# Kernel tuning notes

Hardware: AMD Instinct MI355X
Metric: run time of the kernel (lower is better)

The kernel has to match this reference:

```python
import jax, jax.numpy as jnp
import numpy as np

N = 4096
INPUT_DIM = 256
HIDDEN = 64
HEADS = 8
NEG_SLOPE = 0.2
MASK_FILL = -10000.0


def setup_inputs() -> dict:
    key = jax.random.key(0)
    k_x, k_adj, k_w, k_as, k_ad = jax.random.split(key, 5)
    x = jax.random.normal(k_x, (N, INPUT_DIM), dtype=jnp.float32)
    adjacency = jax.random.bernoulli(k_adj, 0.05, (N, N)) | jnp.eye(N, dtype=bool)
    # linear weight, torch convention: [out_features, in_features]
    W = jax.random.normal(k_w, (HEADS * HIDDEN, INPUT_DIM), dtype=jnp.float32) * 0.05
    attn_src = jax.random.normal(k_as, (HEADS, HIDDEN), dtype=jnp.float32) * 0.1
    attn_dst = jax.random.normal(k_ad, (HEADS, HIDDEN), dtype=jnp.float32) * 0.1
    return {"x": x, "adjacency": adjacency, "W": W, "attn_src": attn_src, "attn_dst": attn_dst}


def reference(x, adjacency, W, attn_src, attn_dst):
    # h: [N, heads, hidden]
    h = (x @ W.T).reshape(N, HEADS, HIDDEN)
    src_scores = jnp.einsum('nhd,hd->nh', h, attn_src)  # [N, heads]
    dst_scores = jnp.einsum('nhd,hd->nh', h, attn_dst)  # [N, heads]
    # logits[i, j, h] = src[i, h] + dst[j, h]  (matches torch permute(2,0,1) layout math)
    logits = src_scores[:, None, :] + dst_scores[None, :, :]  # [N, N, heads]
    logits = jax.nn.leaky_relu(logits, negative_slope=NEG_SLOPE)
    logits = jnp.where(adjacency[:, :, None], logits, MASK_FILL)
    alpha = jax.nn.softmax(logits, axis=1)  # softmax over source nodes j
    out = jnp.einsum('ijh,jhf->ihf', alpha, h)  # [N, heads, hidden]
    return out.mean(axis=1)  # [N, hidden]
```

## Files before the change

### kernel.cpp

```cpp
#include <hip/hip_runtime.h>

#define NN 4096
#define IN_DIM 256
#define HID 64
#define HEADS 8

typedef __attribute__((ext_vector_type(4))) float f32x4;
typedef __attribute__((ext_vector_type(8))) short s16x8;
typedef unsigned short u16;
typedef unsigned long long u64;

__device__ inline u16 f2bf(float f) {
  union { float f; unsigned u; } v; v.f = f;
  unsigned r = (v.u + 0x7FFFu + ((v.u >> 16) & 1u)) >> 16;
  return (u16)r;
}
__device__ inline float bf2f(u16 b) {
  union { unsigned u; float f; } v; v.u = ((unsigned)b) << 16;
  return v.f;
}
__device__ __forceinline__ unsigned cvt_pk_bf16(float a, float b) {
  unsigned r;
  asm("v_cvt_pk_bf16_f32 %0, %1, %2" : "=v"(r) : "v"(a), "v"(b));
  return r;
}

__global__ __launch_bounds__(256) void gat_pack(
    const void* __restrict__ adj, u64* __restrict__ bits)
{
  __shared__ int smode;
  const int t = threadIdx.x;
  if (t < 64) {
    const unsigned char* a8 = (const unsigned char*)adj;
    const int* a32 = (const int*)adj;
    size_t i8 = (size_t)(4 * t + 1) * 4097;
    int p8 = a8[i8] != 0;
    size_t k = (size_t)(2 * t + 1);
    int p32 = a32[k * 4097] != 0;
    int p64 = a32[2 * k * 4097] != 0;
    int ok8 = __all(p8), ok32 = __all(p32), ok64 = __all(p64);
    if (t == 0) smode = ok8 ? 0 : (ok32 ? 1 : (ok64 ? 2 : 1));
  }
  __syncthreads();
  const int mode = smode;

  const int lane = t & 63;
  const int wave = (blockIdx.x * blockDim.x + t) >> 6;
  const int nwaves = (gridDim.x * blockDim.x) >> 6;
  const size_t nwords = (size_t)NN * NN / 64;

  for (size_t w = wave; w < nwords; w += nwaves) {
    size_t e = w * 64 + lane;
    int on;
    if (mode == 1)      on = ((const int*)adj)[e] != 0;
    else if (mode == 0) on = ((const unsigned char*)adj)[e] != 0;
    else                on = ((const long long*)adj)[e] != 0;
    u64 b = __ballot(on);
    if (lane == 0) bits[w] = b;
  }
}

__global__ __launch_bounds__(256) void gat_gemm1(
    const float* __restrict__ x, const float* __restrict__ W,
    const float* __restrict__ a_src, const float* __restrict__ a_dst,
    u16* __restrict__ Hbt, float* __restrict__ s_srcT,
    float* __restrict__ s_dstT)
{
  __shared__ u16 xhi[64 * 72], xlo[64 * 72], whi[64 * 72], wlo[64 * 72];
  const int nb = blockIdx.x;
  const int ob = blockIdx.y;
  const int t = threadIdx.x;
  const int lane = t & 63, wid = t >> 6;
  const int wr = wid >> 1, wc = wid & 1;
  const int g = lane >> 4;

  f32x4 acc[2][2] = {};

  const int sn = t >> 2;
  const int skc = (t & 3) * 16;

  for (int kb = 0; kb < 4; ++kb) {
    const float* xr = x + (size_t)(nb * 64 + sn) * IN_DIM + kb * 64 + skc;
    const float* wr_p = W + (size_t)(ob * 64 + sn) * IN_DIM + kb * 64 + skc;
#pragma unroll
    for (int c = 0; c < 4; ++c) {
      float4 xv = ((const float4*)xr)[c];
      float4 wv = ((const float4*)wr_p)[c];
      float xf[4] = {xv.x, xv.y, xv.z, xv.w};
      float wf[4] = {wv.x, wv.y, wv.z, wv.w};
      u16 xh[4], xl[4], wh[4], wl[4];
#pragma unroll
      for (int e = 0; e < 4; ++e) {
        xh[e] = f2bf(xf[e]); xl[e] = f2bf(xf[e] - bf2f(xh[e]));
        wh[e] = f2bf(wf[e]); wl[e] = f2bf(wf[e] - bf2f(wh[e]));
      }
      int base = sn * 72 + skc + c * 4;
      *(ushort4*)(xhi + base) = make_ushort4(xh[0], xh[1], xh[2], xh[3]);
      *(ushort4*)(xlo + base) = make_ushort4(xl[0], xl[1], xl[2], xl[3]);
      *(ushort4*)(whi + base) = make_ushort4(wh[0], wh[1], wh[2], wh[3]);
      *(ushort4*)(wlo + base) = make_ushort4(wl[0], wl[1], wl[2], wl[3]);
    }
    __syncthreads();
#pragma unroll
    for (int ks = 0; ks < 2; ++ks) {
      const int k0 = ks * 32 + g * 8;
      s16x8 ah[2], al[2], bh[2], bl[2];
#pragma unroll
      for (int nf = 0; nf < 2; ++nf) {
        int row = wr * 32 + nf * 16 + (lane & 15);
        ah[nf] = *(const s16x8*)(xhi + row * 72 + k0);
        al[nf] = *(const s16x8*)(xlo + row * 72 + k0);
      }
#pragma unroll
      for (int of = 0; of < 2; ++of) {
        int row = wc * 32 + of * 16 + (lane & 15);
        bh[of] = *(const s16x8*)(whi + row * 72 + k0);
        bl[of] = *(const s16x8*)(wlo + row * 72 + k0);
      }
#pragma unroll
      for (int nf = 0; nf < 2; ++nf)
#pragma unroll
        for (int of = 0; of < 2; ++of) {
          acc[nf][of] = __builtin_amdgcn_mfma_f32_16x16x32_bf16(ah[nf], bh[of], acc[nf][of], 0, 0, 0);
          acc[nf][of] = __builtin_amdgcn_mfma_f32_16x16x32_bf16(ah[nf], bl[of], acc[nf][of], 0, 0, 0);
          acc[nf][of] = __builtin_amdgcn_mfma_f32_16x16x32_bf16(al[nf], bh[of], acc[nf][of], 0, 0, 0);
        }
    }
    __syncthreads();
  }

  u16* Ct = xhi;
#pragma unroll
  for (int nf = 0; nf < 2; ++nf)
#pragma unroll
    for (int of = 0; of < 2; ++of)
#pragma unroll
      for (int r = 0; r < 4; ++r) {
        int nloc = wr * 32 + nf * 16 + g * 4 + r;
        int oloc = wc * 32 + of * 16 + (lane & 15);
        Ct[oloc * 72 + nloc] = f2bf(acc[nf][of][r]);
      }

  {
    const float* asp = a_src + ob * 64;
    const float* adp = a_dst + ob * 64;
    float as0 = asp[wc * 32 + (lane & 15)], as1 = asp[wc * 32 + 16 + (lane & 15)];
    float ad0 = adp[wc * 32 + (lane & 15)], ad1 = adp[wc * 32 + 16 + (lane & 15)];
    float* sred = (float*)wlo;
#pragma unroll
    for (int nf = 0; nf < 2; ++nf)
#pragma unroll
      for (int r = 0; r < 4; ++r) {
        float vs = acc[nf][0][r] * as0 + acc[nf][1][r] * as1;
        float vd = acc[nf][0][r] * ad0 + acc[nf][1][r] * ad1;
#pragma unroll
        for (int m = 1; m < 16; m <<= 1) { vs += __shfl_xor(vs, m); vd += __shfl_xor(vd, m); }
        if ((lane & 15) == 0) {
          int node = wr * 32 + nf * 16 + g * 4 + r;
          sred[wc * 64 + node] = vs;
          sred[128 + wc * 64 + node] = vd;
        }
      }
  }
  __syncthreads();
  {
    int o = t >> 2, nc = (t & 3) * 16;
    u16* dst = Hbt + ((size_t)(ob * 64 + nb) * 64 + o) * 64 + nc;
#pragma unroll
    for (int c = 0; c < 2; ++c) {
      s16x8 v = *(const s16x8*)(Ct + o * 72 + nc + c * 8);
      *(s16x8*)(dst + c * 8) = v;
    }
  }
  if (t < 64) {
    const float* sred = (const float*)wlo;
    s_srcT[(size_t)ob * NN + nb * 64 + t] = sred[t] + sred[64 + t];
    s_dstT[(size_t)ob * NN + nb * 64 + t] = sred[128 + t] + sred[192 + t];
  }
}

__global__ __launch_bounds__(512) void gat_dmax(
    const float* __restrict__ s_dstT, float* __restrict__ Mh)
{
  const int w = threadIdx.x >> 6, lane = threadIdx.x & 63;
  const float* p = s_dstT + (size_t)w * NN;
  float m = -INFINITY;
#pragma unroll
  for (int it = 0; it < 16; ++it) {
    f32x4 v = *(const f32x4*)(p + (it * 64 + lane) * 4);
    m = fmaxf(fmaxf(fmaxf(m, v[0]), v[1]), fmaxf(v[2], v[3]));
  }
#pragma unroll
  for (int s = 1; s < 64; s <<= 1) m = fmaxf(m, __shfl_xor(m, s));
  if (lane == 0) Mh[w] = m;
}

__global__ __launch_bounds__(512, 4) void gat_flash(
    const u64* __restrict__ bits, const u16* __restrict__ Hbt,
    const float* __restrict__ s_srcT, const float* __restrict__ s_dstT,
    const float* __restrict__ Mh, float* __restrict__ pout)
{
  __shared__ char shmem[32768];
  __shared__ float Lbuf[8][16];
  u16* Ast = (u16*)shmem;

  const int t = threadIdx.x, lane = t & 63, wid = t >> 6;
  const int ws4 = wid & 3, jh = wid >> 2;
  const int bid = blockIdx.x;
  const int h = bid & 7, iblk = bid >> 3;
  const int i_loc = lane & 15, g = lane >> 4, j0 = g * 8;
  const int irow = iblk * 64 + ws4 * 16 + i_loc;

  const float s_i = s_srcT[(size_t)h * NN + irow];
  float m_i = s_i + Mh[h];
  m_i = fmaxf(m_i, 0.2f * m_i);
  const float L2E = 1.44269504f;
  const float mL = m_i * L2E;

  const u16* tile0 = Hbt + (size_t)h * 64 * 4096;
  const float* dT = s_dstT + (size_t)h * NN;
  const u64* brow = bits + (size_t)irow * 64;

  const int lt = t & 255;
  const int r0 = lt >> 3, colE = (lt & 7) * 8;
  const u16* gsrc0 = tile0 + r0 * 64 + (colE ^ ((r0 & 7) << 3));
  const u16* gsrc1 = tile0 + (32 + r0) * 64 + (colE ^ ((r0 & 7) << 3));
  u16* sgrp = Ast + jh * 8192;
  const int swz = (i_loc & 7) << 4;

  f32x4 acc[4] = {};
  f32x4 lacc = {0.f, 0.f, 0.f, 0.f};

#define QUAD(DV, MBITS, SH, PW0, PW1, LI) do {                        \
    float z0 = s_i + DV[0], z1 = s_i + DV[1];                         \
    float z2 = s_i + DV[2], z3 = s_i + DV[3];                         \
    z0 = fmaxf(z0, 0.2f * z0); z1 = fmaxf(z1, 0.2f * z1);             \
    z2 = fmaxf(z2, 0.2f * z2); z3 = fmaxf(z3, 0.2f * z3);             \
    float e0 = __builtin_amdgcn_exp2f(__builtin_fmaf(z0, L2E, -mL));  \
    float e1 = __builtin_amdgcn_exp2f(__builtin_fmaf(z1, L2E, -mL));  \
    float e2 = __builtin_amdgcn_exp2f(__builtin_fmaf(z2, L2E, -mL));  \
    float e3 = __builtin_amdgcn_exp2f(__builtin_fmaf(z3, L2E, -mL));  \
    e0 = ((MBITS >> (SH + 0)) & 1u) ? e0 : 0.f;                       \
    e1 = ((MBITS >> (SH + 1)) & 1u) ? e1 : 0.f;                       \
    e2 = ((MBITS >> (SH + 2)) & 1u) ? e2 : 0.f;                       \
    e3 = ((MBITS >> (SH + 3)) & 1u) ? e3 : 0.f;                       \
    lacc[LI] += (e0 + e1) + (e2 + e3);                                \
    PW0 = cvt_pk_bf16(e0, e1); PW1 = cvt_pk_bf16(e2, e3);             \
  } while (0)

  const int jtb = jh * 32;
  s16x8 sv0 = *(const s16x8*)(gsrc0 + jtb * 4096);
  s16x8 sv1 = *(const s16x8*)(gsrc1 + jtb * 4096);

  for (int it = 0; it < 32; ++it) {
    const int jt = jtb + it;
    u16* sdst = sgrp + (it & 1) * 4096;

    *(s16x8*)(sdst + lt * 8) = sv0;
    *(s16x8*)(sdst + 2048 + lt * 8) = sv1;
    if (it < 31) {
      sv0 = *(const s16x8*)(gsrc0 + (jt + 1) * 4096);
      sv1 = *(const s16x8*)(gsrc1 + (jt + 1) * 4096);
    }

    const u64 am_ = brow[jt];
    const float* dp = dT + jt * 64 + j0;
    f32x4 d0 = *(const f32x4*)(dp);
    f32x4 d1 = *(const f32x4*)(dp + 4);
    f32x4 d2 = *(const f32x4*)(dp + 32);
    f32x4 d3 = *(const f32x4*)(dp + 36);
    const unsigned amlo = (unsigned)(am_ >> j0);
    const unsigned amhi = (unsigned)(am_ >> (32 + j0));
    union { unsigned w_[4]; s16x8 v_; } P0, P1;
    QUAD(d0, amlo, 0, P0.w_[0], P0.w_[1], 0);
    QUAD(d1, amlo, 4, P0.w_[2], P0.w_[3], 1);
    QUAD(d2, amhi, 0, P1.w_[0], P1.w_[1], 2);
    QUAD(d3, amhi, 4, P1.w_[2], P1.w_[3], 3);

    __syncthreads();

    const char* lbase = (const char*)sdst;
#pragma unroll
    for (int fb = 0; fb < 4; ++fb) {
      const int rowb = (fb * 16 + i_loc) * 128;
      s16x8 A0 = *(const s16x8*)(lbase + rowb + ((g * 16) ^ swz));
      s16x8 A1 = *(const s16x8*)(lbase + rowb + (((g * 16) + 64) ^ swz));
      acc[fb] = __builtin_amdgcn_mfma_f32_16x16x32_bf16(A0, P0.v_, acc[fb], 0, 0, 0);
      acc[fb] = __builtin_amdgcn_mfma_f32_16x16x32_bf16(A1, P1.v_, acc[fb], 0, 0, 0);
    }
  }
#undef QUAD

  float l_run = (lacc[0] + lacc[1]) + (lacc[2] + lacc[3]);
  l_run += __shfl_xor(l_run, 16);
  l_run += __shfl_xor(l_run, 32);
  if (lane < 16) Lbuf[wid][i_loc] = l_run;

  __syncthreads();
  float* accst = (float*)shmem;
  if (jh == 1) {
    float* ab = accst + (ws4 * 16 + i_loc) * 66;
#pragma unroll
    for (int fb = 0; fb < 4; ++fb)
      *(f32x4*)(ab + fb * 16 + g * 4) = acc[fb];
  }
  __syncthreads();
  if (jh == 0) {
    const float invL = 1.f / (l_run + Lbuf[4 + ws4][i_loc]);
    float* ob = pout + ((size_t)h * NN + irow) * 64;
#pragma unroll
    for (int fb = 0; fb < 4; ++fb) {
      f32x4 v = acc[fb] +
          *(const f32x4*)(accst + (ws4 * 16 + i_loc) * 66 + fb * 16 + g * 4);
      *(f32x4*)(ob + fb * 16 + g * 4) = v * invL;
    }
  }
}

__global__ __launch_bounds__(256) void gat_combine(
    const float* __restrict__ pout, float* __restrict__ out)
{
  size_t e = (size_t)blockIdx.x * 256 + threadIdx.x;
  f32x4 s = {0.f, 0.f, 0.f, 0.f};
#pragma unroll
  for (int h = 0; h < 8; ++h)
    s += ((const f32x4*)pout)[(size_t)h * (NN * 16) + e];
  ((f32x4*)out)[e] = s * 0.125f;
}

extern "C" void kernel_launch(void* const* d_in, const int* in_sizes, int n_in,
                              void* d_out, int out_size, void* d_ws, size_t ws_size,
                              hipStream_t stream)
{
  const float* x = (const float*)d_in[0];
  const void* adj = d_in[1];
  const float* W = (const float*)d_in[2];
  const float* a_src = (const float*)d_in[3];
  const float* a_dst = (const float*)d_in[4];
  float* out = (float*)d_out;

  char* ws = (char*)d_ws;
  float* pout = (float*)ws;
  u16* Hbt = (u16*)(ws + 8 * 1024 * 1024);
  float* s_srcT = (float*)(ws + 12 * 1024 * 1024);
  float* s_dstT = (float*)(ws + 12 * 1024 * 1024 + 128 * 1024);
  float* Mh = (float*)(ws + 12 * 1024 * 1024 + 384 * 1024);
  u64* bits = (u64*)(ws + 12 * 1024 * 1024 + 512 * 1024);

  gat_pack<<<2048, 256, 0, stream>>>(adj, bits);
  gat_gemm1<<<dim3(64, 8), 256, 0, stream>>>(x, W, a_src, a_dst, Hbt, s_srcT, s_dstT);
  gat_dmax<<<1, 512, 0, stream>>>(s_dstT, Mh);
  gat_flash<<<512, 512, 0, stream>>>(bits, Hbt, s_srcT, s_dstT, Mh, pout);
  gat_combine<<<256, 256, 0, stream>>>(pout, out);
}
```

Baseline: 90.16 us.

## Hoist bf16 split of x/W into pack kernel and fuse dst-max via atomics

The fp32-to-bf16 hi/lo split of x and W moves out of the GEMM into the adjacency-packing kernel, and the GEMM now loads pre-split bf16 tiles. The separate single-block dst-max kernel is removed: each GEMM block reduces its dst scores and applies an atomicMax on an order-preserving unsigned encoding. This drops one kernel launch and the redundant per-tile conversions in the GEMM, at the cost of extra global traffic for the split copies and atomic contention. The workspace for the split arrays overlaps pout, which is only written later by the flash kernel.

Measured after the change: 91.02 us. Within noise of the previous version (+1.0%).

```diff
diff --git a/kernel.cpp b/kernel.cpp
--- a/kernel.cpp
+++ b/kernel.cpp
@@ -24,12 +24,47 @@
   asm("v_cvt_pk_bf16_f32 %0, %1, %2" : "=v"(r) : "v"(a), "v"(b));
   return r;
 }
-
-__global__ __launch_bounds__(256) void gat_pack(
-    const void* __restrict__ adj, u64* __restrict__ bits)
-{
+__device__ inline unsigned encf(float f) {
+  unsigned u = __float_as_uint(f);
+  return (u & 0x80000000u) ? ~u : (u | 0x80000000u);
+}
+__device__ inline float decf(unsigned k) {
+  return (k & 0x80000000u) ? __uint_as_float(k & 0x7FFFFFFFu) : __uint_as_float(~k);
+}
+
+__global__ __launch_bounds__(256) void gat_prep(
+    const void* __restrict__ adj, const float* __restrict__ x,
+    const float* __restrict__ W, u64* __restrict__ bits,
+    u16* __restrict__ xhi_g, u16* __restrict__ xlo_g,
+    u16* __restrict__ whi_g, u16* __restrict__ wlo_g,
+    unsigned* __restrict__ Mh_enc)
+{
+  const int t = threadIdx.x;
+  const int gtid = blockIdx.x * 256 + t;
+  if (blockIdx.x == 0 && t < 8) Mh_enc[t] = 0u;
+
+  if (gtid < 262144) {
+    f32x4 v = ((const f32x4*)x)[gtid];
+    ushort4 hi, lo;
+    hi.x = f2bf(v[0]); lo.x = f2bf(v[0] - bf2f(hi.x));
+    hi.y = f2bf(v[1]); lo.y = f2bf(v[1] - bf2f(hi.y));
+    hi.z = f2bf(v[2]); lo.z = f2bf(v[2] - bf2f(hi.z));
+    hi.w = f2bf(v[3]); lo.w = f2bf(v[3] - bf2f(hi.w));
+    ((ushort4*)xhi_g)[gtid] = hi;
+    ((ushort4*)xlo_g)[gtid] = lo;
+  }
+  if (gtid < 32768) {
+    f32x4 v = ((const f32x4*)W)[gtid];
+    ushort4 hi, lo;
+    hi.x = f2bf(v[0]); lo.x = f2bf(v[0] - bf2f(hi.x));
+    hi.y = f2bf(v[1]); lo.y = f2bf(v[1] - bf2f(hi.y));
+    hi.z = f2bf(v[2]); lo.z = f2bf(v[2] - bf2f(hi.z));
+    hi.w = f2bf(v[3]); lo.w = f2bf(v[3] - bf2f(hi.w));
+    ((ushort4*)whi_g)[gtid] = hi;
+    ((ushort4*)wlo_g)[gtid] = lo;
+  }
+
   __shared__ int smode;
-  const int t = threadIdx.x;
   if (t < 64) {
     const unsigned char* a8 = (const unsigned char*)adj;
     const int* a32 = (const int*)adj;
@@ -48,7 +83,6 @@
   const int wave = (blockIdx.x * blockDim.x + t) >> 6;
   const int nwaves = (gridDim.x * blockDim.x) >> 6;
   const size_t nwords = (size_t)NN * NN / 64;
-
   for (size_t w = wave; w < nwords; w += nwaves) {
     size_t e = w * 64 + lane;
     int on;
@@ -61,10 +95,11 @@
 }
 
 __global__ __launch_bounds__(256) void gat_gemm1(
-    const float* __restrict__ x, const float* __restrict__ W,
+    const u16* __restrict__ xhi_g, const u16* __restrict__ xlo_g,
+    const u16* __restrict__ whi_g, const u16* __restrict__ wlo_g,
     const float* __restrict__ a_src, const float* __restrict__ a_dst,
     u16* __restrict__ Hbt, float* __restrict__ s_srcT,
-    float* __restrict__ s_dstT)
+    float* __restrict__ s_dstT, unsigned* __restrict__ Mh_enc)
 {
   __shared__ u16 xhi[64 * 72], xlo[64 * 72], whi[64 * 72], wlo[64 * 72];
   const int nb = blockIdx.x;
@@ -80,26 +115,19 @@
   const int skc = (t & 3) * 16;
 
   for (int kb = 0; kb < 4; ++kb) {
-    const float* xr = x + (size_t)(nb * 64 + sn) * IN_DIM + kb * 64 + skc;
-    const float* wr_p = W + (size_t)(ob * 64 + sn) * IN_DIM + kb * 64 + skc;
-#pragma unroll
-    for (int c = 0; c < 4; ++c) {
-      float4 xv = ((const float4*)xr)[c];
-      float4 wv = ((const float4*)wr_p)[c];
-      float xf[4] = {xv.x, xv.y, xv.z, xv.w};
-      float wf[4] = {wv.x, wv.y, wv.z, wv.w};
-      u16 xh[4], xl[4], wh[4], wl[4];
-#pragma unroll
-      for (int e = 0; e < 4; ++e) {
-        xh[e] = f2bf(xf[e]); xl[e] = f2bf(xf[e] - bf2f(xh[e]));
-        wh[e] = f2bf(wf[e]); wl[e] = f2bf(wf[e] - bf2f(wh[e]));
-      }
-      int base = sn * 72 + skc + c * 4;
-      *(ushort4*)(xhi + base) = make_ushort4(xh[0], xh[1], xh[2], xh[3]);
-      *(ushort4*)(xlo + base) = make_ushort4(xl[0], xl[1], xl[2], xl[3]);
-      *(ushort4*)(whi + base) = make_ushort4(wh[0], wh[1], wh[2], wh[3]);
-      *(ushort4*)(wlo + base) = make_ushort4(wl[0], wl[1], wl[2], wl[3]);
-    }
+    const u16* xh_p = xhi_g + (size_t)(nb * 64 + sn) * IN_DIM + kb * 64 + skc;
+    const u16* xl_p = xlo_g + (size_t)(nb * 64 + sn) * IN_DIM + kb * 64 + skc;
+    const u16* wh_p = whi_g + (size_t)(ob * 64 + sn) * IN_DIM + kb * 64 + skc;
+    const u16* wl_p = wlo_g + (size_t)(ob * 64 + sn) * IN_DIM + kb * 64 + skc;
+    const int base = sn * 72 + skc;
+    *(s16x8*)(xhi + base)     = *(const s16x8*)(xh_p);
+    *(s16x8*)(xhi + base + 8) = *(const s16x8*)(xh_p + 8);
+    *(s16x8*)(xlo + base)     = *(const s16x8*)(xl_p);
+    *(s16x8*)(xlo + base + 8) = *(const s16x8*)(xl_p + 8);
+    *(s16x8*)(whi + base)     = *(const s16x8*)(wh_p);
+    *(s16x8*)(whi + base + 8) = *(const s16x8*)(wh_p + 8);
+    *(s16x8*)(wlo + base)     = *(const s16x8*)(wl_p);
+    *(s16x8*)(wlo + base + 8) = *(const s16x8*)(wl_p + 8);
     __syncthreads();
 #pragma unroll
     for (int ks = 0; ks < 2; ++ks) {
@@ -174,31 +202,21 @@
   }
   if (t < 64) {
     const float* sred = (const float*)wlo;
-    s_srcT[(size_t)ob * NN + nb * 64 + t] = sred[t] + sred[64 + t];
-    s_dstT[(size_t)ob * NN + nb * 64 + t] = sred[128 + t] + sred[192 + t];
-  }
-}
-
-__global__ __launch_bounds__(512) void gat_dmax(
-    const float* __restrict__ s_dstT, float* __restrict__ Mh)
-{
-  const int w = threadIdx.x >> 6, lane = threadIdx.x & 63;
-  const float* p = s_dstT + (size_t)w * NN;
-  float m = -INFINITY;
-#pragma unroll
-  for (int it = 0; it < 16; ++it) {
-    f32x4 v = *(const f32x4*)(p + (it * 64 + lane) * 4);
-    m = fmaxf(fmaxf(fmaxf(m, v[0]), v[1]), fmaxf(v[2], v[3]));
-  }
-#pragma unroll
-  for (int s = 1; s < 64; s <<= 1) m = fmaxf(m, __shfl_xor(m, s));
-  if (lane == 0) Mh[w] = m;
+    float vssum = sred[t] + sred[64 + t];
+    float vdsum = sred[128 + t] + sred[192 + t];
+    s_srcT[(size_t)ob * NN + nb * 64 + t] = vssum;
+    s_dstT[(size_t)ob * NN + nb * 64 + t] = vdsum;
+    float m = vdsum;
+#pragma unroll
+    for (int s = 1; s < 64; s <<= 1) m = fmaxf(m, __shfl_xor(m, s));
+    if (t == 0) atomicMax(Mh_enc + ob, encf(m));
+  }
 }
 
 __global__ __launch_bounds__(512, 4) void gat_flash(
     const u64* __restrict__ bits, const u16* __restrict__ Hbt,
     const float* __restrict__ s_srcT, const float* __restrict__ s_dstT,
-    const float* __restrict__ Mh, float* __restrict__ pout)
+    const unsigned* __restrict__ Mh_enc, float* __restrict__ pout)
 {
   __shared__ char shmem[32768];
   __shared__ float Lbuf[8][16];
@@ -212,7 +230,7 @@
   const int irow = iblk * 64 + ws4 * 16 + i_loc;
 
   const float s_i = s_srcT[(size_t)h * NN + irow];
-  float m_i = s_i + Mh[h];
+  float m_i = s_i + decf(Mh_enc[h]);
   m_i = fmaxf(m_i, 0.2f * m_i);
   const float L2E = 1.44269504f;
   const float mL = m_i * L2E;
@@ -340,16 +358,20 @@
   float* out = (float*)d_out;
 
   char* ws = (char*)d_ws;
+  u16* xhi_g = (u16*)ws;
+  u16* xlo_g = (u16*)(ws + 2 * 1024 * 1024);
+  u16* whi_g = (u16*)(ws + 4 * 1024 * 1024);
+  u16* wlo_g = (u16*)(ws + 4 * 1024 * 1024 + 256 * 1024);
   float* pout = (float*)ws;
   u16* Hbt = (u16*)(ws + 8 * 1024 * 1024);
   float* s_srcT = (float*)(ws + 12 * 1024 * 1024);
   float* s_dstT = (float*)(ws + 12 * 1024 * 1024 + 128 * 1024);
-  float* Mh = (float*)(ws + 12 * 1024 * 1024 + 384 * 1024);
+  unsigned* Mh_enc = (unsigned*)(ws + 12 * 1024 * 1024 + 384 * 1024);
   u64* bits = (u64*)(ws + 12 * 1024 * 1024 + 512 * 1024);
 
-  gat_pack<<<2048, 256, 0, stream>>>(adj, bits);
-  gat_gemm1<<<dim3(64, 8), 256, 0, stream>>>(x, W, a_src, a_dst, Hbt, s_srcT, s_dstT);
-  gat_dmax<<<1, 512, 0, stream>>>(s_dstT, Mh);
-  gat_flash<<<512, 512, 0, stream>>>(bits, Hbt, s_srcT, s_dstT, Mh, pout);
+  gat_prep<<<2048, 256, 0, stream>>>(adj, x, W, bits, xhi_g, xlo_g, whi_g, wlo_g, Mh_enc);
+  gat_gemm1<<<dim3(64, 8), 256, 0, stream>>>(xhi_g, xlo_g, whi_g, wlo_g,
+                                             a_src, a_dst, Hbt, s_srcT, s_dstT, Mh_enc);
+  gat_flash<<<512, 512, 0, stream>>>(bits, Hbt, s_srcT, s_dstT, Mh_enc, pout);
   gat_combine<<<256, 256, 0, stream>>>(pout, out);
 }
```
